# Performance work log

Measured on AMD Instinct MI355X. Metric: run time of the kernel, lower is better.

Reference implementation:

```python
import jax, jax.numpy as jnp
import numpy as np

N = 50000   # nodes
E = 800000  # edges (avg degree 16)
F = 96      # num_features
H = 96      # hidden_channels
G = 64      # graphs in batch
ALPHA = 0.5


def setup_inputs() -> dict:
    key = jax.random.key(0)
    ks = jax.random.split(key, 32)
    inp = {
        "x": jax.random.normal(ks[0], (N, F), jnp.float32),
        "edge_index": jax.random.randint(ks[1], (2, E), 0, N, dtype=jnp.int32),
        "batch": jnp.sort(jax.random.randint(ks[2], (N,), 0, G, dtype=jnp.int32)),
    }
    i = 3
    dims = [(F, H), (H, H), (H, H)]
    for l, (din, dout) in enumerate(dims, start=1):
        for tag in ("Wself", "Wsd", "Wds"):
            inp[f"{tag}{l}"] = jax.random.normal(ks[i], (din, dout), jnp.float32) * 0.05; i += 1
        for tag in ("bself", "bsd", "bds"):
            inp[f"{tag}{l}"] = jax.random.normal(ks[i], (dout,), jnp.float32) * 0.05; i += 1
    inp["lin1_w"] = jax.random.normal(ks[i], (H, 5), jnp.float32) * 0.05; i += 1
    inp["lin1_b"] = jax.random.normal(ks[i], (5,), jnp.float32) * 0.05; i += 1
    inp["lin2_w"] = jax.random.normal(ks[i], (5, 1), jnp.float32) * 0.05; i += 1
    inp["lin2_b"] = jax.random.normal(ks[i], (1,), jnp.float32) * 0.05
    return inp


def _agg_mean(x, idx_from, idx_to, n):
    # scatter-mean of x[idx_from] onto idx_to (PyG SAGEConv mean aggregation;
    # nodes with no incoming edges get 0)
    s = jax.ops.segment_sum(x[idx_from], idx_to, num_segments=n)
    c = jax.ops.segment_sum(jnp.ones((idx_to.shape[0],), x.dtype), idx_to, num_segments=n)
    return s / jnp.maximum(c, 1.0)[:, None]


def _dir_sage(x, src, dst, Wself, bself, Wsd, bsd, Wds, bds):
    n = x.shape[0]
    out_self = x @ Wself + bself
    # source_to_target: aggregate x[src] at dst; target_to_source: aggregate x[dst] at src
    out_sd = _agg_mean(x, src, dst, n) @ Wsd + bsd
    out_ds = _agg_mean(x, dst, src, n) @ Wds + bds
    return out_self + (1.0 - ALPHA) * out_sd + ALPHA * out_ds


def reference(x, edge_index, batch,
              Wself1, bself1, Wsd1, bsd1, Wds1, bds1,
              Wself2, bself2, Wsd2, bsd2, Wds2, bds2,
              Wself3, bself3, Wsd3, bsd3, Wds3, bds3,
              lin1_w, lin1_b, lin2_w, lin2_b):
    src, dst = edge_index[0], edge_index[1]
    h = jax.nn.relu(_dir_sage(x, src, dst, Wself1, bself1, Wsd1, bsd1, Wds1, bds1))
    h = jax.nn.relu(_dir_sage(h, src, dst, Wself2, bself2, Wsd2, bsd2, Wds2, bds2))
    h = jax.nn.relu(_dir_sage(h, src, dst, Wself3, bself3, Wsd3, bsd3, Wds3, bds3))
    g = jax.ops.segment_max(h, batch, num_segments=G)  # global_max_pool -> [G, H]
    g = jax.nn.relu(g @ lin1_w + lin1_b)
    return g @ lin2_w + lin2_b  # [G, 1]
```

## Files before the change

kernel.cpp:

```cpp
#include <hip/hip_runtime.h>
#include <hip/hip_bf16.h>

#define HF 96
#define GG 64
#define DEG 64
#define CAPB 4608

typedef __attribute__((ext_vector_type(8))) short bf16x8;
typedef __attribute__((ext_vector_type(4))) float f32x4;
typedef unsigned int uint;

__device__ __forceinline__ unsigned short f2bf(float f) {
    unsigned u = __float_as_uint(f);
    unsigned r = (u + 0x7FFFu + ((u >> 16) & 1u)) >> 16;
    return (unsigned short)r;
}
__device__ __forceinline__ float bf2f(unsigned short h) {
    return __uint_as_float(((unsigned)h) << 16);
}

__device__ __forceinline__ uint4 pack_hilo4(float f0, float f1, float f2, float f3) {
    unsigned short h0 = f2bf(f0), h1 = f2bf(f1), h2 = f2bf(f2), h3 = f2bf(f3);
    unsigned short l0 = f2bf(f0 - bf2f(h0)), l1 = f2bf(f1 - bf2f(h1));
    unsigned short l2 = f2bf(f2 - bf2f(h2)), l3 = f2bf(f3 - bf2f(h3));
    uint4 o;
    o.x = (uint)h0 | ((uint)h1 << 16);
    o.y = (uint)h2 | ((uint)h3 << 16);
    o.z = (uint)l0 | ((uint)l1 << 16);
    o.w = (uint)l2 | ((uint)l3 << 16);
    return o;
}

__device__ __forceinline__ void acc_hilo4(float4& a, uint4 w) {
    a.x += __uint_as_float(w.x << 16) + __uint_as_float(w.z << 16);
    a.y += __uint_as_float(w.x & 0xFFFF0000u) + __uint_as_float(w.z & 0xFFFF0000u);
    a.z += __uint_as_float(w.y << 16) + __uint_as_float(w.w << 16);
    a.w += __uint_as_float(w.y & 0xFFFF0000u) + __uint_as_float(w.w & 0xFFFF0000u);
}

__global__ __launch_bounds__(256) void build_phase1(
        const float* __restrict__ x, const int* __restrict__ ei,
        unsigned short* __restrict__ Ag,
        uint* __restrict__ pcnt, uint* __restrict__ pq, unsigned* __restrict__ g,
        const float* Ws1, const float* Wsd1, const float* Wds1,
        const float* bs1, const float* bsd1, const float* bds1,
        const float* Ws2, const float* Wsd2, const float* Wds2,
        const float* bs2, const float* bsd2, const float* bds2,
        const float* Ws3, const float* Wsd3, const float* Wds3,
        const float* bs3, const float* bsd3, const float* bds3,
        unsigned short* __restrict__ Whi3, unsigned short* __restrict__ Wlo3,
        float* __restrict__ bc3, int N, int E, int NB, int CE) {
    if (blockIdx.x < 256) {
        __shared__ int hist[512];
        __shared__ int lbase[512];
        for (int i = threadIdx.x; i < NB; i += 256) hist[i] = 0;
        __syncthreads();
        const int e0 = blockIdx.x * CE;
        int e1 = e0 + CE; if (e1 > E) e1 = E;
        for (int e = e0 + threadIdx.x; e < e1; e += 256) {
            int s = ei[e], d = ei[E + e];
            atomicAdd(&hist[d >> 8], 1);
            atomicAdd(&hist[(N + s) >> 8], 1);
        }
        __syncthreads();
        for (int b = threadIdx.x; b < NB; b += 256) {
            int h = hist[b];
            lbase[b] = h ? (int)atomicAdd(&pcnt[b], (uint)h) : 0;
        }
        __syncthreads();
        for (int e = e0 + threadIdx.x; e < e1; e += 256) {
            int s = ei[e], d = ei[E + e];
            int b0 = d >> 8;
            int p0 = atomicAdd(&lbase[b0], 1);
            if (p0 < CAPB) pq[(long long)b0 * CAPB + p0] = ((uint)(d & 255) << 16) | (uint)s;
            int k1 = N + s;
            int b1 = k1 >> 8;
            int p1 = atomicAdd(&lbase[b1], 1);
            if (p1 < CAPB) pq[(long long)b1 * CAPB + p1] = ((uint)(k1 & 255) << 16) | (uint)d;
        }
        return;
    }
    int t = (blockIdx.x - 256) * 256 + threadIdx.x;
    const int R0 = N * 24;
    if (t < R0) {
        int n = t / 24, q = t % 24;
        float4 v = *(const float4*)(x + (long long)n * HF + q * 4);
        *(uint4*)(Ag + ((long long)n * 576 + q * 8)) = pack_hilo4(v.x, v.y, v.z, v.w);
        return;
    }
    t -= R0;
    if (t < GG * HF) { g[t] = 0u; return; }
    t -= GG * HF;
    const int PER = HF * 288 + HF;
    if (t >= 3 * PER) return;
    int l = t / PER;
    int idx = t % PER;
    const float* Wself = (l == 0) ? Ws1 : (l == 1) ? Ws2 : Ws3;
    const float* Wsd   = (l == 0) ? Wsd1 : (l == 1) ? Wsd2 : Wsd3;
    const float* Wds   = (l == 0) ? Wds1 : (l == 1) ? Wds2 : Wds3;
    const float* bself = (l == 0) ? bs1 : (l == 1) ? bs2 : bs3;
    const float* bsd   = (l == 0) ? bsd1 : (l == 1) ? bsd2 : bsd3;
    const float* bds   = (l == 0) ? bds1 : (l == 1) ? bds2 : bds3;
    unsigned short* Whi = Whi3 + (long long)l * HF * 288;
    unsigned short* Wlo = Wlo3 + (long long)l * HF * 288;
    float* bc = bc3 + l * HF;
    if (idx < HF * 288) {
        int j = idx / 288;
        int kk = idx % 288;
        int m = kk / HF, k = kk % HF;
        const float* W = (m == 0) ? Wself : (m == 1) ? Wsd : Wds;
        float w = W[k * HF + j];
        unsigned short hi = f2bf(w);
        Whi[idx] = hi;
        Wlo[idx] = f2bf(w - bf2f(hi));
    } else {
        int j = idx - HF * 288;
        bc[j] = bself[j] + 0.5f * (bsd[j] + bds[j]);
    }
}

__global__ __launch_bounds__(256) void build_phase2(
        const uint* __restrict__ pcnt, const uint* __restrict__ pq,
        int* __restrict__ cnt, int* __restrict__ nbr, int N) {
    int b = blockIdx.x;
    __shared__ int lcnt[256];
    lcnt[threadIdx.x] = 0;
    __syncthreads();
    int tot = (int)pcnt[b]; if (tot > CAPB) tot = CAPB;
    const uint* q = pq + (long long)b * CAPB;
    for (int i = threadIdx.x; i < tot; i += 256) {
        uint p = q[i];
        int lk = (int)(p >> 16);
        int v = (int)(p & 0xFFFFu);
        int slot = atomicAdd(&lcnt[lk], 1);
        long long k = ((long long)b << 8) + lk;
        if (slot < DEG) nbr[(k << 6) + slot] = v;
    }
    __syncthreads();
    long long k = ((long long)b << 8) + threadIdx.x;
    if (k < 2LL * N) cnt[k] = lcnt[threadIdx.x];
}

__global__ __launch_bounds__(256) void gather_kernel(
        unsigned short* Ag, const int* __restrict__ cnt, const int* __restrict__ nbr, int N) {
    int t = blockIdx.x * blockDim.x + threadIdx.x;
    int P = t / 24;
    if (P >= 2 * N) return;
    int q = t % 24;
    int dir = (P >= N) ? 1 : 0;
    int n = P - dir * N;

    int degt = cnt[P];
    int deg = (degt > DEG) ? DEG : degt;
    const int* nb = nbr + ((long long)P << 6);

    const unsigned short* xq = Ag + q * 8;
    float4 a0 = make_float4(0.f, 0.f, 0.f, 0.f);
    float4 a1 = a0, a2 = a0, a3 = a0;
    int i = 0;
    for (; i + 4 <= deg; i += 4) {
        int i0 = nb[i + 0], i1 = nb[i + 1], i2 = nb[i + 2], i3 = nb[i + 3];
        uint4 w0 = *(const uint4*)(xq + (long long)i0 * 576);
        uint4 w1 = *(const uint4*)(xq + (long long)i1 * 576);
        uint4 w2 = *(const uint4*)(xq + (long long)i2 * 576);
        uint4 w3 = *(const uint4*)(xq + (long long)i3 * 576);
        acc_hilo4(a0, w0);
        acc_hilo4(a1, w1);
        acc_hilo4(a2, w2);
        acc_hilo4(a3, w3);
    }
    for (; i < deg; i++) {
        uint4 w0 = *(const uint4*)(xq + (long long)nb[i] * 576);
        acc_hilo4(a0, w0);
    }
    float4 acc;
    acc.x = (a0.x + a1.x) + (a2.x + a3.x);
    acc.y = (a0.y + a1.y) + (a2.y + a3.y);
    acc.z = (a0.z + a1.z) + (a2.z + a3.z);
    acc.w = (a0.w + a1.w) + (a2.w + a3.w);
    float inv = 0.5f / fmaxf((float)degt, 1.0f);
    acc.x *= inv; acc.y *= inv; acc.z *= inv; acc.w *= inv;
    int chunk = 24 + dir * 24 + q;
    *(uint4*)(Ag + ((long long)n * 576 + chunk * 8)) = pack_hilo4(acc.x, acc.y, acc.z, acc.w);
}

#define LPAD 40
__global__ __launch_bounds__(256) void sage_mfma(
        unsigned short* Ag,
        const unsigned short* __restrict__ Whi_g, const unsigned short* __restrict__ Wlo_g,
        const float* __restrict__ bc, const int* __restrict__ batch,
        unsigned* __restrict__ gmax, int mode, int N) {
    __shared__ __align__(16) unsigned char POOL[25600];
    unsigned short* Ahi = (unsigned short*)POOL;
    unsigned short* Alo = Ahi + 64 * LPAD;
    unsigned short* Whi = Alo + 64 * LPAD;
    unsigned short* Wlo = Whi + 96 * LPAD;
    float* C = (float*)POOL;

    const int tx = threadIdx.x;
    const int lane = tx & 63;
    const int wid = tx >> 6;
    const int wr = (wid >> 1) * 32;
    const int wc = (wid & 1) * 48;
    const int m = lane & 15;
    const int quad = lane >> 4;
    const int row0 = blockIdx.x * 64;

    const int arow = tx >> 2;
    const int aj = tx & 3;
    int argc = row0 + arow; if (argc > N - 1) argc = N - 1;
    const unsigned short* Arow = Ag + (long long)argc * 576;

    f32x4 acc[2][3];
#pragma unroll
    for (int rt = 0; rt < 2; rt++)
#pragma unroll
        for (int ct = 0; ct < 3; ct++) acc[rt][ct] = (f32x4){0.f, 0.f, 0.f, 0.f};

    for (int kt = 0; kt < 9; kt++) {
        const int kglob = kt * 32;

        {
            const uint4 v0 = *(const uint4*)(Arow + (kt * 8 + aj * 2 + 0) * 8);
            const uint4 v1 = *(const uint4*)(Arow + (kt * 8 + aj * 2 + 1) * 8);
            *(uint2*)&Ahi[arow * LPAD + aj * 8 + 0] = make_uint2(v0.x, v0.y);
            *(uint2*)&Alo[arow * LPAD + aj * 8 + 0] = make_uint2(v0.z, v0.w);
            *(uint2*)&Ahi[arow * LPAD + aj * 8 + 4] = make_uint2(v1.x, v1.y);
            *(uint2*)&Alo[arow * LPAD + aj * 8 + 4] = make_uint2(v1.z, v1.w);
        }
        for (int s = tx; s < 384; s += 256) {
            int n = s >> 2, q2 = s & 3;
            long long go = (long long)n * 288 + kglob + q2 * 8;
            *(bf16x8*)&Whi[n * LPAD + q2 * 8] = *(const bf16x8*)(Whi_g + go);
            *(bf16x8*)&Wlo[n * LPAD + q2 * 8] = *(const bf16x8*)(Wlo_g + go);
        }
        __syncthreads();

        bf16x8 ah[2], al[2], bh[3], bl[3];
#pragma unroll
        for (int rt = 0; rt < 2; rt++) {
            int r = (wr + rt * 16 + m) * LPAD + quad * 8;
            ah[rt] = *(const bf16x8*)&Ahi[r];
            al[rt] = *(const bf16x8*)&Alo[r];
        }
#pragma unroll
        for (int ct = 0; ct < 3; ct++) {
            int r = (wc + ct * 16 + m) * LPAD + quad * 8;
            bh[ct] = *(const bf16x8*)&Whi[r];
            bl[ct] = *(const bf16x8*)&Wlo[r];
        }
#pragma unroll
        for (int rt = 0; rt < 2; rt++)
#pragma unroll
            for (int ct = 0; ct < 3; ct++) {
                acc[rt][ct] = __builtin_amdgcn_mfma_f32_16x16x32_bf16(ah[rt], bh[ct], acc[rt][ct], 0, 0, 0);
                acc[rt][ct] = __builtin_amdgcn_mfma_f32_16x16x32_bf16(ah[rt], bl[ct], acc[rt][ct], 0, 0, 0);
                acc[rt][ct] = __builtin_amdgcn_mfma_f32_16x16x32_bf16(al[rt], bh[ct], acc[rt][ct], 0, 0, 0);
            }
        __syncthreads();
    }

#pragma unroll
    for (int ct = 0; ct < 3; ct++) {
        int col = wc + ct * 16 + m;
        float bcv = bc[col];
#pragma unroll
        for (int rt = 0; rt < 2; rt++) {
#pragma unroll
            for (int reg = 0; reg < 4; reg++) {
                int rl = wr + rt * 16 + quad * 4 + reg;
                C[rl * 100 + col] = fmaxf(acc[rt][ct][reg] + bcv, 0.f);
            }
        }
    }
    __syncthreads();

    if (mode == 0) {
        int rl = tx >> 2;
        int r = row0 + rl;
        if (r < N) {
            unsigned short* Orow = Ag + (long long)r * 576;
#pragma unroll
            for (int k = 0; k < 6; k++) {
                int c = aj * 6 + k;
                const float* src = &C[rl * 100 + c * 4];
                *(uint4*)(Orow + c * 8) = pack_hilo4(src[0], src[1], src[2], src[3]);
            }
        }
    } else {
        if (tx < HF) {
            int j = tx;
            int rmax = N - row0; if (rmax > 64) rmax = 64;
            float cur = 0.0f;
            int curb = -1;
            for (int r = 0; r < rmax; r++) {
                int bt = batch[row0 + r];
                float v = C[r * 100 + j];
                if (bt != curb) {
                    if (curb >= 0) atomicMax(&gmax[curb * HF + j], __float_as_uint(cur));
                    curb = bt;
                    cur = v;
                } else {
                    cur = fmaxf(cur, v);
                }
            }
            if (curb >= 0) atomicMax(&gmax[curb * HF + j], __float_as_uint(cur));
        }
    }
}

__global__ void mlp_kernel(const unsigned* __restrict__ g, const float* __restrict__ lin1_w,
                           const float* __restrict__ lin1_b, const float* __restrict__ lin2_w,
                           const float* __restrict__ lin2_b, float* __restrict__ out) {
    int gi = threadIdx.x;
    if (gi >= GG) return;
    float h5[5];
#pragma unroll
    for (int hh = 0; hh < 5; hh++) {
        float acc = lin1_b[hh];
#pragma unroll 8
        for (int k = 0; k < HF; k++)
            acc = fmaf(__uint_as_float(g[gi * HF + k]), lin1_w[k * 5 + hh], acc);
        h5[hh] = fmaxf(acc, 0.0f);
    }
    float o = lin2_b[0];
#pragma unroll
    for (int hh = 0; hh < 5; hh++) o = fmaf(h5[hh], lin2_w[hh * 1 + 0], o);
    out[gi] = o;
}

extern "C" void kernel_launch(void* const* d_in, const int* in_sizes, int n_in,
                              void* d_out, int out_size, void* d_ws, size_t ws_size,
                              hipStream_t stream) {
    const float* x     = (const float*)d_in[0];
    const int*   ei    = (const int*)d_in[1];
    const int*   batch = (const int*)d_in[2];
    const float* W[3][3];
    const float* B[3][3];
    for (int l = 0; l < 3; l++) {
        for (int t = 0; t < 3; t++) W[l][t] = (const float*)d_in[3 + l * 6 + t];
        for (int t = 0; t < 3; t++) B[l][t] = (const float*)d_in[3 + l * 6 + 3 + t];
    }
    const float* lin1_w = (const float*)d_in[21];
    const float* lin1_b = (const float*)d_in[22];
    const float* lin2_w = (const float*)d_in[23];
    const float* lin2_b = (const float*)d_in[24];

    const int N = in_sizes[0] / HF;
    const int E = in_sizes[1] / 2;
    const int NB = (2 * N + 255) / 256;
    const int CE = (E + 255) / 256;

    unsigned short* Ag = (unsigned short*)d_ws;
    int* cnt = (int*)(Ag + (long long)N * 576);
    int* nbr = cnt + 2LL * N;
    uint* pcnt = (uint*)(nbr + 2LL * N * DEG);
    uint* pq = pcnt + NB;
    float* bc3 = (float*)(pq + (long long)NB * CAPB);
    uintptr_t p = (uintptr_t)(bc3 + 3 * HF);
    p = (p + 15) & ~(uintptr_t)15;
    unsigned short* Whi3 = (unsigned short*)p;
    unsigned short* Wlo3 = Whi3 + 3 * HF * 288;
    uintptr_t p2 = (uintptr_t)(Wlo3 + 3 * HF * 288);
    p2 = (p2 + 15) & ~(uintptr_t)15;
    unsigned* g = (unsigned*)p2;

    hipMemsetAsync(pcnt, 0, (size_t)NB * sizeof(uint), stream);

    const long long lin_threads = (long long)N * 24 + GG * HF + 3LL * (HF * 288 + HF);
    const int lin_blocks = (int)((lin_threads + 255) / 256);
    build_phase1<<<256 + lin_blocks, 256, 0, stream>>>(
        x, ei, Ag, pcnt, pq, g,
        W[0][0], W[0][1], W[0][2], B[0][0], B[0][1], B[0][2],
        W[1][0], W[1][1], W[1][2], B[1][0], B[1][1], B[1][2],
        W[2][0], W[2][1], W[2][2], B[2][0], B[2][1], B[2][2],
        Whi3, Wlo3, bc3, N, E, NB, CE);
    build_phase2<<<NB, 256, 0, stream>>>(pcnt, pq, cnt, nbr, N);

    const long long gather_threads = (long long)2 * N * 24;
    const int gather_blocks = (int)((gather_threads + 255) / 256);
    const int gemm_blocks = (N + 63) / 64;

    for (int l = 0; l < 3; l++) {
        gather_kernel<<<gather_blocks, 256, 0, stream>>>(Ag, cnt, nbr, N);
        sage_mfma<<<gemm_blocks, 256, 0, stream>>>(
            Ag,
            Whi3 + (long long)l * HF * 288, Wlo3 + (long long)l * HF * 288,
            bc3 + l * HF, batch, g, (l < 2) ? 0 : 1, N);
    }

    mlp_kernel<<<1, 64, 0, stream>>>(g, lin1_w, lin1_b, lin2_w, lin2_b, (float*)d_out);
}
```

Baseline: 464.0 us.

## Split node features from aggregates and feed MFMA operands directly from global

The single 576-element-per-node buffer becomes two buffers: a compact 192-element hi/lo feature buffer that the gather reads, and a separate 384-element buffer for the two directional aggregates. The neighbour gather now touches a much smaller, denser array, which should improve cache hit rates on random-index loads. The GEMM kernel drops LDS staging and its per-k-step barriers, loading A and W fragments straight from global memory into MFMA registers. This relies on L1/L2 to serve the repeated W reads and may suffer from less coalesced A loads. The output is still written in place into hbuf while being declared __restrict__ against the input.

```diff
diff --git a/kernel.cpp b/kernel.cpp
--- a/kernel.cpp
+++ b/kernel.cpp
@@ -5,10 +5,14 @@
 #define GG 64
 #define DEG 64
 #define CAPB 4608
+#define CPAD 100
 
 typedef __attribute__((ext_vector_type(8))) short bf16x8;
 typedef __attribute__((ext_vector_type(4))) float f32x4;
+typedef __attribute__((ext_vector_type(4))) unsigned int uint4v;
 typedef unsigned int uint;
+
+union BFU { uint4v u; bf16x8 b; };
 
 __device__ __forceinline__ unsigned short f2bf(float f) {
     unsigned u = __float_as_uint(f);
@@ -40,7 +44,7 @@
 
 __global__ __launch_bounds__(256) void build_phase1(
         const float* __restrict__ x, const int* __restrict__ ei,
-        unsigned short* __restrict__ Ag,
+        unsigned short* __restrict__ hbuf,
         uint* __restrict__ pcnt, uint* __restrict__ pq, unsigned* __restrict__ g,
         const float* Ws1, const float* Wsd1, const float* Wds1,
         const float* bs1, const float* bsd1, const float* bds1,
@@ -85,7 +89,7 @@
     if (t < R0) {
         int n = t / 24, q = t % 24;
         float4 v = *(const float4*)(x + (long long)n * HF + q * 4);
-        *(uint4*)(Ag + ((long long)n * 576 + q * 8)) = pack_hilo4(v.x, v.y, v.z, v.w);
+        *(uint4*)(hbuf + ((long long)n * 192 + q * 8)) = pack_hilo4(v.x, v.y, v.z, v.w);
         return;
     }
     t -= R0;
@@ -142,7 +146,8 @@
 }
 
 __global__ __launch_bounds__(256) void gather_kernel(
-        unsigned short* Ag, const int* __restrict__ cnt, const int* __restrict__ nbr, int N) {
+        const unsigned short* __restrict__ hbuf, unsigned short* __restrict__ abuf,
+        const int* __restrict__ cnt, const int* __restrict__ nbr, int N) {
     int t = blockIdx.x * blockDim.x + threadIdx.x;
     int P = t / 24;
     if (P >= 2 * N) return;
@@ -154,23 +159,23 @@
     int deg = (degt > DEG) ? DEG : degt;
     const int* nb = nbr + ((long long)P << 6);
 
-    const unsigned short* xq = Ag + q * 8;
+    const unsigned short* xq = hbuf + q * 8;
     float4 a0 = make_float4(0.f, 0.f, 0.f, 0.f);
     float4 a1 = a0, a2 = a0, a3 = a0;
     int i = 0;
     for (; i + 4 <= deg; i += 4) {
         int i0 = nb[i + 0], i1 = nb[i + 1], i2 = nb[i + 2], i3 = nb[i + 3];
-        uint4 w0 = *(const uint4*)(xq + (long long)i0 * 576);
-        uint4 w1 = *(const uint4*)(xq + (long long)i1 * 576);
-        uint4 w2 = *(const uint4*)(xq + (long long)i2 * 576);
-        uint4 w3 = *(const uint4*)(xq + (long long)i3 * 576);
+        uint4 w0 = *(const uint4*)(xq + (long long)i0 * 192);
+        uint4 w1 = *(const uint4*)(xq + (long long)i1 * 192);
+        uint4 w2 = *(const uint4*)(xq + (long long)i2 * 192);
+        uint4 w3 = *(const uint4*)(xq + (long long)i3 * 192);
         acc_hilo4(a0, w0);
         acc_hilo4(a1, w1);
         acc_hilo4(a2, w2);
         acc_hilo4(a3, w3);
     }
     for (; i < deg; i++) {
-        uint4 w0 = *(const uint4*)(xq + (long long)nb[i] * 576);
+        uint4 w0 = *(const uint4*)(xq + (long long)nb[i] * 192);
         acc_hilo4(a0, w0);
     }
     float4 acc;
@@ -180,22 +185,17 @@
     acc.w = (a0.w + a1.w) + (a2.w + a3.w);
     float inv = 0.5f / fmaxf((float)degt, 1.0f);
     acc.x *= inv; acc.y *= inv; acc.z *= inv; acc.w *= inv;
-    int chunk = 24 + dir * 24 + q;
-    *(uint4*)(Ag + ((long long)n * 576 + chunk * 8)) = pack_hilo4(acc.x, acc.y, acc.z, acc.w);
-}
-
-#define LPAD 40
+    *(uint4*)(abuf + ((long long)n * 384 + (dir * 24 + q) * 8)) =
+        pack_hilo4(acc.x, acc.y, acc.z, acc.w);
+}
+
 __global__ __launch_bounds__(256) void sage_mfma(
-        unsigned short* Ag,
+        const unsigned short* __restrict__ hbuf, const unsigned short* __restrict__ abuf,
+        unsigned short* __restrict__ hout,
         const unsigned short* __restrict__ Whi_g, const unsigned short* __restrict__ Wlo_g,
         const float* __restrict__ bc, const int* __restrict__ batch,
         unsigned* __restrict__ gmax, int mode, int N) {
-    __shared__ __align__(16) unsigned char POOL[25600];
-    unsigned short* Ahi = (unsigned short*)POOL;
-    unsigned short* Alo = Ahi + 64 * LPAD;
-    unsigned short* Whi = Alo + 64 * LPAD;
-    unsigned short* Wlo = Whi + 96 * LPAD;
-    float* C = (float*)POOL;
+    __shared__ __align__(16) float C[64 * CPAD];
 
     const int tx = threadIdx.x;
     const int lane = tx & 63;
@@ -206,10 +206,19 @@
     const int quad = lane >> 4;
     const int row0 = blockIdx.x * 64;
 
-    const int arow = tx >> 2;
-    const int aj = tx & 3;
-    int argc = row0 + arow; if (argc > N - 1) argc = N - 1;
-    const unsigned short* Arow = Ag + (long long)argc * 576;
+    int rA[2];
+#pragma unroll
+    for (int rt = 0; rt < 2; rt++) {
+        int r = row0 + wr + rt * 16 + m;
+        rA[rt] = (r < N) ? r : (N - 1);
+    }
+    const unsigned short* hrow0 = hbuf + (long long)rA[0] * 192;
+    const unsigned short* hrow1 = hbuf + (long long)rA[1] * 192;
+    const unsigned short* arow0 = abuf + (long long)rA[0] * 384;
+    const unsigned short* arow1 = abuf + (long long)rA[1] * 384;
+    long long wbase[3];
+#pragma unroll
+    for (int ct = 0; ct < 3; ct++) wbase[ct] = (long long)(wc + ct * 16 + m) * 288 + quad * 8;
 
     f32x4 acc[2][3];
 #pragma unroll
@@ -217,48 +226,40 @@
 #pragma unroll
         for (int ct = 0; ct < 3; ct++) acc[rt][ct] = (f32x4){0.f, 0.f, 0.f, 0.f};
 
-    for (int kt = 0; kt < 9; kt++) {
-        const int kglob = kt * 32;
-
-        {
-            const uint4 v0 = *(const uint4*)(Arow + (kt * 8 + aj * 2 + 0) * 8);
-            const uint4 v1 = *(const uint4*)(Arow + (kt * 8 + aj * 2 + 1) * 8);
-            *(uint2*)&Ahi[arow * LPAD + aj * 8 + 0] = make_uint2(v0.x, v0.y);
-            *(uint2*)&Alo[arow * LPAD + aj * 8 + 0] = make_uint2(v0.z, v0.w);
-            *(uint2*)&Ahi[arow * LPAD + aj * 8 + 4] = make_uint2(v1.x, v1.y);
-            *(uint2*)&Alo[arow * LPAD + aj * 8 + 4] = make_uint2(v1.z, v1.w);
-        }
-        for (int s = tx; s < 384; s += 256) {
-            int n = s >> 2, q2 = s & 3;
-            long long go = (long long)n * 288 + kglob + q2 * 8;
-            *(bf16x8*)&Whi[n * LPAD + q2 * 8] = *(const bf16x8*)(Whi_g + go);
-            *(bf16x8*)&Wlo[n * LPAD + q2 * 8] = *(const bf16x8*)(Wlo_g + go);
-        }
-        __syncthreads();
-
-        bf16x8 ah[2], al[2], bh[3], bl[3];
-#pragma unroll
-        for (int rt = 0; rt < 2; rt++) {
-            int r = (wr + rt * 16 + m) * LPAD + quad * 8;
-            ah[rt] = *(const bf16x8*)&Ahi[r];
-            al[rt] = *(const bf16x8*)&Alo[r];
-        }
-#pragma unroll
-        for (int ct = 0; ct < 3; ct++) {
-            int r = (wc + ct * 16 + m) * LPAD + quad * 8;
-            bh[ct] = *(const bf16x8*)&Whi[r];
-            bl[ct] = *(const bf16x8*)&Wlo[r];
-        }
-#pragma unroll
-        for (int rt = 0; rt < 2; rt++)
-#pragma unroll
-            for (int ct = 0; ct < 3; ct++) {
-                acc[rt][ct] = __builtin_amdgcn_mfma_f32_16x16x32_bf16(ah[rt], bh[ct], acc[rt][ct], 0, 0, 0);
-                acc[rt][ct] = __builtin_amdgcn_mfma_f32_16x16x32_bf16(ah[rt], bl[ct], acc[rt][ct], 0, 0, 0);
-                acc[rt][ct] = __builtin_amdgcn_mfma_f32_16x16x32_bf16(al[rt], bh[ct], acc[rt][ct], 0, 0, 0);
-            }
-        __syncthreads();
-    }
+#define KSTEP(PA0, PA1, KOFF) do {                                                   \
+    bf16x8 ah[2], al[2], bh[3], bl[3];                                               \
+    { uint4 v0 = *(const uint4*)(PA0); uint4 v1 = *(const uint4*)((PA0) + 8);        \
+      BFU uh; uh.u = (uint4v){v0.x, v0.y, v1.x, v1.y}; ah[0] = uh.b;                 \
+      BFU ul; ul.u = (uint4v){v0.z, v0.w, v1.z, v1.w}; al[0] = ul.b; }               \
+    { uint4 v0 = *(const uint4*)(PA1); uint4 v1 = *(const uint4*)((PA1) + 8);        \
+      BFU uh; uh.u = (uint4v){v0.x, v0.y, v1.x, v1.y}; ah[1] = uh.b;                 \
+      BFU ul; ul.u = (uint4v){v0.z, v0.w, v1.z, v1.w}; al[1] = ul.b; }               \
+    _Pragma("unroll")                                                                \
+    for (int ct = 0; ct < 3; ct++) {                                                 \
+        bh[ct] = *(const bf16x8*)(Whi_g + wbase[ct] + (KOFF));                       \
+        bl[ct] = *(const bf16x8*)(Wlo_g + wbase[ct] + (KOFF));                       \
+    }                                                                                \
+    _Pragma("unroll")                                                                \
+    for (int rt = 0; rt < 2; rt++)                                                   \
+        _Pragma("unroll")                                                            \
+        for (int ct = 0; ct < 3; ct++) {                                             \
+            acc[rt][ct] = __builtin_amdgcn_mfma_f32_16x16x32_bf16(ah[rt], bh[ct], acc[rt][ct], 0, 0, 0); \
+            acc[rt][ct] = __builtin_amdgcn_mfma_f32_16x16x32_bf16(ah[rt], bl[ct], acc[rt][ct], 0, 0, 0); \
+            acc[rt][ct] = __builtin_amdgcn_mfma_f32_16x16x32_bf16(al[rt], bh[ct], acc[rt][ct], 0, 0, 0); \
+        }                                                                            \
+} while (0)
+
+#pragma unroll
+    for (int kt = 0; kt < 3; kt++)
+        KSTEP(hrow0 + (kt * 8 + quad * 2) * 8, hrow1 + (kt * 8 + quad * 2) * 8, kt * 32);
+#pragma unroll
+    for (int kt = 0; kt < 3; kt++)
+        KSTEP(arow0 + (kt * 8 + quad * 2) * 8, arow1 + (kt * 8 + quad * 2) * 8, 96 + kt * 32);
+#pragma unroll
+    for (int kt = 0; kt < 3; kt++)
+        KSTEP(arow0 + 192 + (kt * 8 + quad * 2) * 8, arow1 + 192 + (kt * 8 + quad * 2) * 8,
+              192 + kt * 32);
+#undef KSTEP
 
 #pragma unroll
     for (int ct = 0; ct < 3; ct++) {
@@ -269,7 +270,7 @@
 #pragma unroll
             for (int reg = 0; reg < 4; reg++) {
                 int rl = wr + rt * 16 + quad * 4 + reg;
-                C[rl * 100 + col] = fmaxf(acc[rt][ct][reg] + bcv, 0.f);
+                C[rl * CPAD + col] = fmaxf(acc[rt][ct][reg] + bcv, 0.f);
             }
         }
     }
@@ -277,13 +278,14 @@
 
     if (mode == 0) {
         int rl = tx >> 2;
+        int aj = tx & 3;
         int r = row0 + rl;
         if (r < N) {
-            unsigned short* Orow = Ag + (long long)r * 576;
+            unsigned short* Orow = hout + (long long)r * 192;
 #pragma unroll
             for (int k = 0; k < 6; k++) {
                 int c = aj * 6 + k;
-                const float* src = &C[rl * 100 + c * 4];
+                const float* src = &C[rl * CPAD + c * 4];
                 *(uint4*)(Orow + c * 8) = pack_hilo4(src[0], src[1], src[2], src[3]);
             }
         }
@@ -295,7 +297,7 @@
             int curb = -1;
             for (int r = 0; r < rmax; r++) {
                 int bt = batch[row0 + r];
-                float v = C[r * 100 + j];
+                float v = C[r * CPAD + j];
                 if (bt != curb) {
                     if (curb >= 0) atomicMax(&gmax[curb * HF + j], __float_as_uint(cur));
                     curb = bt;
@@ -351,8 +353,9 @@
     const int NB = (2 * N + 255) / 256;
     const int CE = (E + 255) / 256;
 
-    unsigned short* Ag = (unsigned short*)d_ws;
-    int* cnt = (int*)(Ag + (long long)N * 576);
+    unsigned short* hbuf = (unsigned short*)d_ws;
+    unsigned short* abuf = hbuf + (long long)N * 192;
+    int* cnt = (int*)(abuf + (long long)N * 384);
     int* nbr = cnt + 2LL * N;
     uint* pcnt = (uint*)(nbr + 2LL * N * DEG);
     uint* pq = pcnt + NB;
@@ -370,7 +373,7 @@
     const long long lin_threads = (long long)N * 24 + GG * HF + 3LL * (HF * 288 + HF);
     const int lin_blocks = (int)((lin_threads + 255) / 256);
     build_phase1<<<256 + lin_blocks, 256, 0, stream>>>(
-        x, ei, Ag, pcnt, pq, g,
+        x, ei, hbuf, pcnt, pq, g,
         W[0][0], W[0][1], W[0][2], B[0][0], B[0][1], B[0][2],
         W[1][0], W[1][1], W[1][2], B[1][0], B[1][1], B[1][2],
         W[2][0], W[2][1], W[2][2], B[2][0], B[2][1], B[2][2],
@@ -382,9 +385,9 @@
     const int gemm_blocks = (N + 63) / 64;
 
     for (int l = 0; l < 3; l++) {
-        gather_kernel<<<gather_blocks, 256, 0, stream>>>(Ag, cnt, nbr, N);
+        gather_kernel<<<gather_blocks, 256, 0, stream>>>(hbuf, abuf, cnt, nbr, N);
         sage_mfma<<<gemm_blocks, 256, 0, stream>>>(
-            Ag,
+            hbuf, abuf, hbuf,
             Whi3 + (long long)l * HF * 288, Wlo3 + (long long)l * HF * 288,
             bc3 + l * HF, batch, g, (l < 2) ? 0 : 1, N);
     }
```

Measured after the change: 499.7 us. +7.7%, slower.

## Fuse neighbor gather into per-layer MFMA GEMM with ping-pong feature buffers

Applied to the files above, without the earlier changes.

Merges the separate gather and GEMM kernels into one per-layer kernel. Each block gathers the two directional mean aggregates for its 64 nodes into shared memory and feeds them directly to the MFMA, so the aggregates are never written to or re-read from global memory. Features now live in compact 192-short rows that alternate between two buffers across layers. Self features and weights are loaded straight from global memory instead of being staged in LDS. The trade-offs are gather latency that is no longer overlapped across separate kernels, fewer launched threads doing the gather, and uncoalesced direct weight loads.

```diff
diff --git a/kernel.cpp b/kernel.cpp
--- a/kernel.cpp
+++ b/kernel.cpp
@@ -5,10 +5,14 @@
 #define GG 64
 #define DEG 64
 #define CAPB 4608
+#define TPAD 104
 
 typedef __attribute__((ext_vector_type(8))) short bf16x8;
 typedef __attribute__((ext_vector_type(4))) float f32x4;
+typedef __attribute__((ext_vector_type(4))) unsigned int uint4v;
 typedef unsigned int uint;
+
+union BFU { uint4v u; bf16x8 b; };
 
 __device__ __forceinline__ unsigned short f2bf(float f) {
     unsigned u = __float_as_uint(f);
@@ -40,7 +44,7 @@
 
 __global__ __launch_bounds__(256) void build_phase1(
         const float* __restrict__ x, const int* __restrict__ ei,
-        unsigned short* __restrict__ Ag,
+        unsigned short* __restrict__ buf0,
         uint* __restrict__ pcnt, uint* __restrict__ pq, unsigned* __restrict__ g,
         const float* Ws1, const float* Wsd1, const float* Wds1,
         const float* bs1, const float* bsd1, const float* bds1,
@@ -85,7 +89,7 @@
     if (t < R0) {
         int n = t / 24, q = t % 24;
         float4 v = *(const float4*)(x + (long long)n * HF + q * 4);
-        *(uint4*)(Ag + ((long long)n * 576 + q * 8)) = pack_hilo4(v.x, v.y, v.z, v.w);
+        *(uint4*)(buf0 + ((long long)n * 192 + q * 8)) = pack_hilo4(v.x, v.y, v.z, v.w);
         return;
     }
     t -= R0;
@@ -141,60 +145,48 @@
     if (k < 2LL * N) cnt[k] = lcnt[threadIdx.x];
 }
 
-__global__ __launch_bounds__(256) void gather_kernel(
-        unsigned short* Ag, const int* __restrict__ cnt, const int* __restrict__ nbr, int N) {
-    int t = blockIdx.x * blockDim.x + threadIdx.x;
-    int P = t / 24;
-    if (P >= 2 * N) return;
-    int q = t % 24;
-    int dir = (P >= N) ? 1 : 0;
-    int n = P - dir * N;
-
+__device__ __forceinline__ void gather_dir(
+        const unsigned short* __restrict__ bin,
+        const int* __restrict__ cnt, const int* __restrict__ nbr,
+        int P, int nl, int c4, int N,
+        unsigned short* AggHi, unsigned short* AggLo) {
     int degt = cnt[P];
     int deg = (degt > DEG) ? DEG : degt;
     const int* nb = nbr + ((long long)P << 6);
-
-    const unsigned short* xq = Ag + q * 8;
     float4 a0 = make_float4(0.f, 0.f, 0.f, 0.f);
-    float4 a1 = a0, a2 = a0, a3 = a0;
-    int i = 0;
-    for (; i + 4 <= deg; i += 4) {
-        int i0 = nb[i + 0], i1 = nb[i + 1], i2 = nb[i + 2], i3 = nb[i + 3];
-        uint4 w0 = *(const uint4*)(xq + (long long)i0 * 576);
-        uint4 w1 = *(const uint4*)(xq + (long long)i1 * 576);
-        uint4 w2 = *(const uint4*)(xq + (long long)i2 * 576);
-        uint4 w3 = *(const uint4*)(xq + (long long)i3 * 576);
-        acc_hilo4(a0, w0);
-        acc_hilo4(a1, w1);
-        acc_hilo4(a2, w2);
-        acc_hilo4(a3, w3);
-    }
-    for (; i < deg; i++) {
-        uint4 w0 = *(const uint4*)(xq + (long long)nb[i] * 576);
-        acc_hilo4(a0, w0);
-    }
-    float4 acc;
-    acc.x = (a0.x + a1.x) + (a2.x + a3.x);
-    acc.y = (a0.y + a1.y) + (a2.y + a3.y);
-    acc.z = (a0.z + a1.z) + (a2.z + a3.z);
-    acc.w = (a0.w + a1.w) + (a2.w + a3.w);
+    float4 a1 = a0, a2 = a0, a3 = a0, a4 = a0, a5 = a0;
+    for (int i = 0; i < deg; ++i) {
+        const unsigned short* row = bin + (long long)nb[i] * 192 + c4 * 8;
+        uint4 w0 = *(const uint4*)(row + 0);
+        uint4 w1 = *(const uint4*)(row + 32);
+        uint4 w2 = *(const uint4*)(row + 64);
+        uint4 w3 = *(const uint4*)(row + 96);
+        uint4 w4 = *(const uint4*)(row + 128);
+        uint4 w5 = *(const uint4*)(row + 160);
+        acc_hilo4(a0, w0); acc_hilo4(a1, w1); acc_hilo4(a2, w2);
+        acc_hilo4(a3, w3); acc_hilo4(a4, w4); acc_hilo4(a5, w5);
+    }
     float inv = 0.5f / fmaxf((float)degt, 1.0f);
-    acc.x *= inv; acc.y *= inv; acc.z *= inv; acc.w *= inv;
-    int chunk = 24 + dir * 24 + q;
-    *(uint4*)(Ag + ((long long)n * 576 + chunk * 8)) = pack_hilo4(acc.x, acc.y, acc.z, acc.w);
-}
-
-#define LPAD 40
-__global__ __launch_bounds__(256) void sage_mfma(
-        unsigned short* Ag,
+    float4 aa[6] = {a0, a1, a2, a3, a4, a5};
+#pragma unroll
+    for (int j = 0; j < 6; ++j) {
+        int q = c4 + 4 * j;
+        uint4 pk = pack_hilo4(aa[j].x * inv, aa[j].y * inv, aa[j].z * inv, aa[j].w * inv);
+        *(uint2*)&AggHi[nl * TPAD + q * 4] = make_uint2(pk.x, pk.y);
+        *(uint2*)&AggLo[nl * TPAD + q * 4] = make_uint2(pk.z, pk.w);
+    }
+}
+
+__global__ __launch_bounds__(256, 4) void fused_layer(
+        const unsigned short* __restrict__ bin,
+        unsigned short* __restrict__ bout,
+        const int* __restrict__ cnt, const int* __restrict__ nbr,
         const unsigned short* __restrict__ Whi_g, const unsigned short* __restrict__ Wlo_g,
         const float* __restrict__ bc, const int* __restrict__ batch,
         unsigned* __restrict__ gmax, int mode, int N) {
-    __shared__ __align__(16) unsigned char POOL[25600];
-    unsigned short* Ahi = (unsigned short*)POOL;
-    unsigned short* Alo = Ahi + 64 * LPAD;
-    unsigned short* Whi = Alo + 64 * LPAD;
-    unsigned short* Wlo = Whi + 96 * LPAD;
+    __shared__ __align__(16) unsigned char POOL[2 * 64 * TPAD * 2];
+    unsigned short* AggHi = (unsigned short*)POOL;
+    unsigned short* AggLo = AggHi + 64 * TPAD;
     float* C = (float*)POOL;
 
     const int tx = threadIdx.x;
@@ -206,10 +198,9 @@
     const int quad = lane >> 4;
     const int row0 = blockIdx.x * 64;
 
-    const int arow = tx >> 2;
-    const int aj = tx & 3;
-    int argc = row0 + arow; if (argc > N - 1) argc = N - 1;
-    const unsigned short* Arow = Ag + (long long)argc * 576;
+    const int nl = tx >> 2;
+    const int c4 = tx & 3;
+    const int gn = row0 + nl;
 
     f32x4 acc[2][3];
 #pragma unroll
@@ -217,37 +208,32 @@
 #pragma unroll
         for (int ct = 0; ct < 3; ct++) acc[rt][ct] = (f32x4){0.f, 0.f, 0.f, 0.f};
 
-    for (int kt = 0; kt < 9; kt++) {
-        const int kglob = kt * 32;
-
-        {
-            const uint4 v0 = *(const uint4*)(Arow + (kt * 8 + aj * 2 + 0) * 8);
-            const uint4 v1 = *(const uint4*)(Arow + (kt * 8 + aj * 2 + 1) * 8);
-            *(uint2*)&Ahi[arow * LPAD + aj * 8 + 0] = make_uint2(v0.x, v0.y);
-            *(uint2*)&Alo[arow * LPAD + aj * 8 + 0] = make_uint2(v0.z, v0.w);
-            *(uint2*)&Ahi[arow * LPAD + aj * 8 + 4] = make_uint2(v1.x, v1.y);
-            *(uint2*)&Alo[arow * LPAD + aj * 8 + 4] = make_uint2(v1.z, v1.w);
-        }
-        for (int s = tx; s < 384; s += 256) {
-            int n = s >> 2, q2 = s & 3;
-            long long go = (long long)n * 288 + kglob + q2 * 8;
-            *(bf16x8*)&Whi[n * LPAD + q2 * 8] = *(const bf16x8*)(Whi_g + go);
-            *(bf16x8*)&Wlo[n * LPAD + q2 * 8] = *(const bf16x8*)(Wlo_g + go);
-        }
-        __syncthreads();
-
+    int rA[2];
+#pragma unroll
+    for (int rt = 0; rt < 2; rt++) {
+        int r = row0 + wr + rt * 16 + m;
+        rA[rt] = (r < N) ? r : (N - 1);
+    }
+
+    if (gn < N) gather_dir(bin, cnt, nbr, gn, nl, c4, N, AggHi, AggLo);
+    __syncthreads();
+
+#pragma unroll
+    for (int kt = 0; kt < 3; kt++) {
         bf16x8 ah[2], al[2], bh[3], bl[3];
 #pragma unroll
         for (int rt = 0; rt < 2; rt++) {
-            int r = (wr + rt * 16 + m) * LPAD + quad * 8;
-            ah[rt] = *(const bf16x8*)&Ahi[r];
-            al[rt] = *(const bf16x8*)&Alo[r];
+            const unsigned short* Ar = bin + (long long)rA[rt] * 192 + (kt * 8 + quad * 2) * 8;
+            uint4 v0 = *(const uint4*)Ar;
+            uint4 v1 = *(const uint4*)(Ar + 8);
+            BFU uh; uh.u = (uint4v){v0.x, v0.y, v1.x, v1.y}; ah[rt] = uh.b;
+            BFU ul; ul.u = (uint4v){v0.z, v0.w, v1.z, v1.w}; al[rt] = ul.b;
         }
 #pragma unroll
         for (int ct = 0; ct < 3; ct++) {
-            int r = (wc + ct * 16 + m) * LPAD + quad * 8;
-            bh[ct] = *(const bf16x8*)&Whi[r];
-            bl[ct] = *(const bf16x8*)&Wlo[r];
+            long long wo = (long long)(wc + ct * 16 + m) * 288 + kt * 32 + quad * 8;
+            bh[ct] = *(const bf16x8*)(Whi_g + wo);
+            bl[ct] = *(const bf16x8*)(Wlo_g + wo);
         }
 #pragma unroll
         for (int rt = 0; rt < 2; rt++)
@@ -257,8 +243,62 @@
                 acc[rt][ct] = __builtin_amdgcn_mfma_f32_16x16x32_bf16(ah[rt], bl[ct], acc[rt][ct], 0, 0, 0);
                 acc[rt][ct] = __builtin_amdgcn_mfma_f32_16x16x32_bf16(al[rt], bh[ct], acc[rt][ct], 0, 0, 0);
             }
-        __syncthreads();
-    }
+    }
+
+#pragma unroll
+    for (int kt = 0; kt < 3; kt++) {
+        bf16x8 ah[2], al[2], bh[3], bl[3];
+#pragma unroll
+        for (int rt = 0; rt < 2; rt++) {
+            int r = (wr + rt * 16 + m) * TPAD + kt * 32 + quad * 8;
+            ah[rt] = *(const bf16x8*)&AggHi[r];
+            al[rt] = *(const bf16x8*)&AggLo[r];
+        }
+#pragma unroll
+        for (int ct = 0; ct < 3; ct++) {
+            long long wo = (long long)(wc + ct * 16 + m) * 288 + 96 + kt * 32 + quad * 8;
+            bh[ct] = *(const bf16x8*)(Whi_g + wo);
+            bl[ct] = *(const bf16x8*)(Wlo_g + wo);
+        }
+#pragma unroll
+        for (int rt = 0; rt < 2; rt++)
+#pragma unroll
+            for (int ct = 0; ct < 3; ct++) {
+                acc[rt][ct] = __builtin_amdgcn_mfma_f32_16x16x32_bf16(ah[rt], bh[ct], acc[rt][ct], 0, 0, 0);
+                acc[rt][ct] = __builtin_amdgcn_mfma_f32_16x16x32_bf16(ah[rt], bl[ct], acc[rt][ct], 0, 0, 0);
+                acc[rt][ct] = __builtin_amdgcn_mfma_f32_16x16x32_bf16(al[rt], bh[ct], acc[rt][ct], 0, 0, 0);
+            }
+    }
+    __syncthreads();
+
+    if (gn < N) gather_dir(bin, cnt, nbr, N + gn, nl, c4, N, AggHi, AggLo);
+    __syncthreads();
+
+#pragma unroll
+    for (int kt = 0; kt < 3; kt++) {
+        bf16x8 ah[2], al[2], bh[3], bl[3];
+#pragma unroll
+        for (int rt = 0; rt < 2; rt++) {
+            int r = (wr + rt * 16 + m) * TPAD + kt * 32 + quad * 8;
+            ah[rt] = *(const bf16x8*)&AggHi[r];
+            al[rt] = *(const bf16x8*)&AggLo[r];
+        }
+#pragma unroll
+        for (int ct = 0; ct < 3; ct++) {
+            long long wo = (long long)(wc + ct * 16 + m) * 288 + 192 + kt * 32 + quad * 8;
+            bh[ct] = *(const bf16x8*)(Whi_g + wo);
+            bl[ct] = *(const bf16x8*)(Wlo_g + wo);
+        }
+#pragma unroll
+        for (int rt = 0; rt < 2; rt++)
+#pragma unroll
+            for (int ct = 0; ct < 3; ct++) {
+                acc[rt][ct] = __builtin_amdgcn_mfma_f32_16x16x32_bf16(ah[rt], bh[ct], acc[rt][ct], 0, 0, 0);
+                acc[rt][ct] = __builtin_amdgcn_mfma_f32_16x16x32_bf16(ah[rt], bl[ct], acc[rt][ct], 0, 0, 0);
+                acc[rt][ct] = __builtin_amdgcn_mfma_f32_16x16x32_bf16(al[rt], bh[ct], acc[rt][ct], 0, 0, 0);
+            }
+    }
+    __syncthreads();
 
 #pragma unroll
     for (int ct = 0; ct < 3; ct++) {
@@ -269,7 +309,7 @@
 #pragma unroll
             for (int reg = 0; reg < 4; reg++) {
                 int rl = wr + rt * 16 + quad * 4 + reg;
-                C[rl * 100 + col] = fmaxf(acc[rt][ct][reg] + bcv, 0.f);
+                C[rl * TPAD + col] = fmaxf(acc[rt][ct][reg] + bcv, 0.f);
             }
         }
     }
@@ -277,13 +317,14 @@
 
     if (mode == 0) {
         int rl = tx >> 2;
+        int aj = tx & 3;
         int r = row0 + rl;
         if (r < N) {
-            unsigned short* Orow = Ag + (long long)r * 576;
+            unsigned short* Orow = bout + (long long)r * 192;
 #pragma unroll
             for (int k = 0; k < 6; k++) {
                 int c = aj * 6 + k;
-                const float* src = &C[rl * 100 + c * 4];
+                const float* src = &C[rl * TPAD + c * 4];
                 *(uint4*)(Orow + c * 8) = pack_hilo4(src[0], src[1], src[2], src[3]);
             }
         }
@@ -295,7 +336,7 @@
             int curb = -1;
             for (int r = 0; r < rmax; r++) {
                 int bt = batch[row0 + r];
-                float v = C[r * 100 + j];
+                float v = C[r * TPAD + j];
                 if (bt != curb) {
                     if (curb >= 0) atomicMax(&gmax[curb * HF + j], __float_as_uint(cur));
                     curb = bt;
@@ -351,8 +392,9 @@
     const int NB = (2 * N + 255) / 256;
     const int CE = (E + 255) / 256;
 
-    unsigned short* Ag = (unsigned short*)d_ws;
-    int* cnt = (int*)(Ag + (long long)N * 576);
+    unsigned short* buf0 = (unsigned short*)d_ws;
+    unsigned short* buf1 = buf0 + (long long)N * 192;
+    int* cnt = (int*)(buf1 + (long long)N * 192);
     int* nbr = cnt + 2LL * N;
     uint* pcnt = (uint*)(nbr + 2LL * N * DEG);
     uint* pq = pcnt + NB;
@@ -370,24 +412,23 @@
     const long long lin_threads = (long long)N * 24 + GG * HF + 3LL * (HF * 288 + HF);
     const int lin_blocks = (int)((lin_threads + 255) / 256);
     build_phase1<<<256 + lin_blocks, 256, 0, stream>>>(
-        x, ei, Ag, pcnt, pq, g,
+        x, ei, buf0, pcnt, pq, g,
         W[0][0], W[0][1], W[0][2], B[0][0], B[0][1], B[0][2],
         W[1][0], W[1][1], W[1][2], B[1][0], B[1][1], B[1][2],
         W[2][0], W[2][1], W[2][2], B[2][0], B[2][1], B[2][2],
         Whi3, Wlo3, bc3, N, E, NB, CE);
     build_phase2<<<NB, 256, 0, stream>>>(pcnt, pq, cnt, nbr, N);
 
-    const long long gather_threads = (long long)2 * N * 24;
-    const int gather_blocks = (int)((gather_threads + 255) / 256);
-    const int gemm_blocks = (N + 63) / 64;
-
-    for (int l = 0; l < 3; l++) {
-        gather_kernel<<<gather_blocks, 256, 0, stream>>>(Ag, cnt, nbr, N);
-        sage_mfma<<<gemm_blocks, 256, 0, stream>>>(
-            Ag,
-            Whi3 + (long long)l * HF * 288, Wlo3 + (long long)l * HF * 288,
-            bc3 + l * HF, batch, g, (l < 2) ? 0 : 1, N);
-    }
+    const int layer_blocks = (N + 63) / 64;
+
+    fused_layer<<<layer_blocks, 256, 0, stream>>>(
+        buf0, buf1, cnt, nbr, Whi3, Wlo3, bc3, batch, g, 0, N);
+    fused_layer<<<layer_blocks, 256, 0, stream>>>(
+        buf1, buf0, cnt, nbr,
+        Whi3 + (long long)HF * 288, Wlo3 + (long long)HF * 288, bc3 + HF, batch, g, 0, N);
+    fused_layer<<<layer_blocks, 256, 0, stream>>>(
+        buf0, buf1, cnt, nbr,
+        Whi3 + 2LL * HF * 288, Wlo3 + 2LL * HF * 288, bc3 + 2 * HF, batch, g, 1, N);
 
     mlp_kernel<<<1, 64, 0, stream>>>(g, lin1_w, lin1_b, lin2_w, lin2_b, (float*)d_out);
 }
```

After: 508.8 us. 1.1x slower.
